# Kernel tuning notes

Hardware: AMD Instinct MI355X
Metric: run time of the kernel (lower is better)

The kernel has to match this reference:

```python
import jax, jax.numpy as jnp
import numpy as np

PI = float(np.pi)
LN_EPS = 1e-5
COS_EPS = 1e-6

D_HIDDEN, N_HEADS, D_HEAD, D_MLP = 1024, 16, 64, 4096
B, T = 4, 2048


def _xavier(key, shape):
    # torch xavier_uniform on 3D tensor: fan_in = shape[1]*shape[2]? torch uses
    # fan_in = shape[1] * receptive_field(shape[2:]), fan_out = shape[0] * rf.
    rf = 1
    for s in shape[2:]:
        rf *= s
    fan_in, fan_out = shape[1] * rf, shape[0] * rf
    bound = float(np.sqrt(6.0 / (fan_in + fan_out)))
    return jax.random.uniform(key, shape, jnp.float32, -bound, bound)


def setup_inputs() -> dict:
    key = jax.random.key(0)
    ks = jax.random.split(key, 10)
    x = jax.random.normal(ks[0], (B, T, D_HIDDEN), jnp.float32)
    W_Q = _xavier(ks[1], (N_HEADS, D_HIDDEN, 1))
    W_K = _xavier(ks[2], (N_HEADS, D_HIDDEN, 1))
    W_V = _xavier(ks[3], (N_HEADS, D_HIDDEN, D_HEAD))
    W_O = _xavier(ks[4], (D_HIDDEN, D_HEAD, N_HEADS))
    ln1_w = jnp.ones((D_HIDDEN,), jnp.float32)
    ln1_b = jnp.zeros((D_HIDDEN,), jnp.float32)
    ln2_w = jnp.ones((D_HIDDEN,), jnp.float32)
    ln2_b = jnp.zeros((D_HIDDEN,), jnp.float32)
    s1 = 1.0 / np.sqrt(D_HIDDEN)
    s2 = 1.0 / np.sqrt(D_MLP)
    W1 = jax.random.uniform(ks[5], (D_HIDDEN, D_MLP), jnp.float32, -s1, s1)
    b1 = jax.random.uniform(ks[6], (D_MLP,), jnp.float32, -s1, s1)
    W2 = jax.random.uniform(ks[7], (D_MLP, D_HIDDEN), jnp.float32, -s2, s2)
    b2 = jax.random.uniform(ks[8], (D_HIDDEN,), jnp.float32, -s2, s2)
    return {"x": x, "W_Q": W_Q, "W_K": W_K, "W_V": W_V, "W_O": W_O,
            "ln1_w": ln1_w, "ln1_b": ln1_b, "ln2_w": ln2_w, "ln2_b": ln2_b,
            "W1": W1, "b1": b1, "W2": W2, "b2": b2}


def _layer_norm(x, w, b):
    mu = jnp.mean(x, axis=-1, keepdims=True)
    var = jnp.mean(jnp.square(x - mu), axis=-1, keepdims=True)
    return (x - mu) * jax.lax.rsqrt(var + LN_EPS) * w + b


def _cos_attention(y, W_Q, W_K, W_V, W_O):
    q = jnp.einsum('btd,idh->btih', y, W_Q)  # (B,T,H,1)
    k = jnp.einsum('btd,idh->btih', y, W_K)  # (B,T,H,1)
    V = jnp.einsum('btd,idh->btih', y, W_V)  # (B,T,H,Dh)
    # use_tanh branch
    q = jnp.tanh(q) * (PI / 4)
    k = jnp.tanh(k) * (PI / 4)
    cos_k, sin_k = jnp.cos(k), jnp.sin(k)
    cos_KV = jnp.cumsum(cos_k * V, axis=1)
    sin_KV = jnp.cumsum(sin_k * V, axis=1)
    cos_Q, sin_Q = jnp.cos(q), jnp.sin(q)
    heads = cos_Q * cos_KV + sin_Q * sin_KV  # (B,T,H,Dh)
    # epsilon branch: normalizing denominator
    cos_K = jnp.cumsum(cos_k, axis=1)
    sin_K = jnp.cumsum(sin_k, axis=1)
    denom = cos_Q * cos_K + sin_Q * sin_K + COS_EPS  # (B,T,H,1)
    heads = heads / denom
    return jnp.einsum('dhi,btih->btd', W_O, heads)


def reference(x, W_Q, W_K, W_V, W_O, ln1_w, ln1_b, ln2_w, ln2_b, W1, b1, W2, b2):
    y = _layer_norm(x, ln1_w, ln1_b)
    x = x + _cos_attention(y, W_Q, W_K, W_V, W_O)
    y = _layer_norm(x, ln2_w, ln2_b)
    mlp = jnp.dot(jax.nn.gelu(jnp.dot(y, W1) + b1), W2) + b2
    return x + mlp
```

## Files before the change

kernel.cpp:

```cpp
#include <hip/hip_runtime.h>
#include <hip/hip_bf16.h>
#include <stdint.h>

typedef unsigned short u16;
typedef __attribute__((ext_vector_type(4))) unsigned int u32x4;
typedef __attribute__((ext_vector_type(8))) __bf16 bfx8;
typedef __attribute__((ext_vector_type(4))) float f32x4;

#define PI_F 3.14159265358979323846f

__device__ __forceinline__ float bf2f(u16 u) {
    unsigned v = ((unsigned)u) << 16; float f; __builtin_memcpy(&f, &v, 4); return f;
}
__device__ __forceinline__ u16 f2bf(float f) {
    unsigned u; __builtin_memcpy(&u, &f, 4);
    unsigned r = (u + 0x7fffu + ((u >> 16) & 1u)) >> 16; return (u16)r;
}

__device__ __forceinline__ void glds16(const u16* g, const u16* l) {
    __builtin_amdgcn_global_load_lds(
        (const __attribute__((address_space(1))) unsigned int*)(unsigned long long)g,
        (__attribute__((address_space(3))) unsigned int*)(unsigned int)(unsigned long long)l,
        16, 0, 0);
}

__global__ __launch_bounds__(256)
void tconv_kernel(const float* __restrict__ in, u16* __restrict__ out,
                  int R, int C, long inBatch, long outBatch)
{
    __shared__ float tile[64][65];
    const int tx = threadIdx.x & 63;
    const int ty = threadIdx.x >> 6;
    const int bc = blockIdx.x * 64;
    const int br = blockIdx.y * 64;
    const float* ip = in + (long)blockIdx.z * inBatch;
    u16* op = out + (long)blockIdx.z * outBatch;

    #pragma unroll
    for (int rr = ty; rr < 64; rr += 4) {
        int r = br + rr, c = bc + tx;
        tile[rr][tx] = (r < R && c < C) ? ip[(long)r * C + c] : 0.f;
    }
    __syncthreads();
    #pragma unroll
    for (int rr = ty; rr < 64; rr += 4) {
        int oc = bc + rr;
        int orr = br + tx;
        if (oc < C && orr < R)
            op[(long)oc * R + orr] = f2bf(tile[tx][rr]);
    }
}

template<bool DO_QK>
__global__ __launch_bounds__(256)
void ln_kernel(const float* __restrict__ X, const float* __restrict__ w,
               const float* __restrict__ b, u16* __restrict__ Ybf,
               const float* __restrict__ WQ, const float* __restrict__ WK,
               float* __restrict__ cqA, float* __restrict__ sqA,
               float* __restrict__ ckA, float* __restrict__ skA)
{
    __shared__ float yrow[1024];
    __shared__ float wsum[4], wsq[4];
    const int row = blockIdx.x;
    const int tid = threadIdx.x;
    const int lane = tid & 63;
    const int wv = tid >> 6;

    const float4 xv = ((const float4*)(X + (long)row * 1024))[tid];
    float s  = xv.x + xv.y + xv.z + xv.w;
    float sq = xv.x*xv.x + xv.y*xv.y + xv.z*xv.z + xv.w*xv.w;
    #pragma unroll
    for (int off = 32; off; off >>= 1) {
        s  += __shfl_down(s, off);
        sq += __shfl_down(sq, off);
    }
    if (lane == 0) { wsum[wv] = s; wsq[wv] = sq; }
    __syncthreads();
    const float ts = wsum[0] + wsum[1] + wsum[2] + wsum[3];
    const float tq = wsq[0] + wsq[1] + wsq[2] + wsq[3];
    const float mean = ts * (1.f / 1024.f);
    const float var  = tq * (1.f / 1024.f) - mean * mean;
    const float rstd = rsqrtf(var + 1e-5f);

    const float4 wv4 = ((const float4*)w)[tid];
    const float4 bv4 = ((const float4*)b)[tid];
    const float y0 = (xv.x - mean) * rstd * wv4.x + bv4.x;
    const float y1 = (xv.y - mean) * rstd * wv4.y + bv4.y;
    const float y2 = (xv.z - mean) * rstd * wv4.z + bv4.z;
    const float y3 = (xv.w - mean) * rstd * wv4.w + bv4.w;

    uint2 p;
    p.x = (unsigned)f2bf(y0) | ((unsigned)f2bf(y1) << 16);
    p.y = (unsigned)f2bf(y2) | ((unsigned)f2bf(y3) << 16);
    ((uint2*)(Ybf + (long)row * 1024))[tid] = p;

    if (DO_QK) {
        yrow[tid*4+0] = y0; yrow[tid*4+1] = y1;
        yrow[tid*4+2] = y2; yrow[tid*4+3] = y3;
        __syncthreads();
        #pragma unroll
        for (int i = 0; i < 4; ++i) {
            const int h = wv * 4 + i;
            const float* wqp = WQ + (long)h * 1024;
            const float* wkp = WK + (long)h * 1024;
            float dq = 0.f, dk = 0.f;
            #pragma unroll
            for (int j = 0; j < 16; ++j) {
                const float yv = yrow[lane + 64*j];
                dq = fmaf(yv, wqp[lane + 64*j], dq);
                dk = fmaf(yv, wkp[lane + 64*j], dk);
            }
            #pragma unroll
            for (int off = 32; off; off >>= 1) {
                dq += __shfl_down(dq, off);
                dk += __shfl_down(dk, off);
            }
            if (lane == 0) {
                const float aq = tanhf(dq) * (PI_F * 0.25f);
                const float ak = tanhf(dk) * (PI_F * 0.25f);
                float sv, cv;
                const long o = (long)h * 8192 + row;
                __sincosf(aq, &sv, &cv); cqA[o] = cv; sqA[o] = sv;
                __sincosf(ak, &sv, &cv); ckA[o] = cv; skA[o] = sv;
            }
        }
    }
}

__global__ __launch_bounds__(64)
void scan_kernel(const u16* __restrict__ V,
                 const float* __restrict__ cqA, const float* __restrict__ sqA,
                 const float* __restrict__ ckA, const float* __restrict__ skA,
                 u16* __restrict__ H)
{
    __shared__ u16 vt[64][64];
    __shared__ float lck[64], lsk[64], lrc[64], lrs[64];
    const int b = blockIdx.x >> 4;
    const int h = blockIdx.x & 15;
    const int lane = threadIdx.x;
    const long rowbase = (long)b * 2048;
    const long colbase = (long)h * 64;
    const long qbase = (long)h * 8192 + rowbase;

    float csum = 0.f, ssum = 0.f;
    float carry_c = 0.f, carry_s = 0.f;

    for (int ch = 0; ch < 32; ++ch) {
        const int t0 = ch * 64;
        __syncthreads();
        #pragma unroll
        for (int i = 0; i < 8; ++i) {
            const int tt = i * 8 + (lane >> 3);
            const int c0 = (lane & 7) * 8;
            *(u32x4*)&vt[tt][c0] =
                *(const u32x4*)(V + (rowbase + t0 + tt) * 1024 + colbase + c0);
        }
        {
            const float ck = ckA[qbase + t0 + lane];
            const float sk = skA[qbase + t0 + lane];
            const float cq = cqA[qbase + t0 + lane];
            const float sq = sqA[qbase + t0 + lane];
            float c = ck, sscan = sk;
            #pragma unroll
            for (int off = 1; off < 64; off <<= 1) {
                const float oc = __shfl_up(c, off);
                const float os = __shfl_up(sscan, off);
                if (lane >= off) { c += oc; sscan += os; }
            }
            const float cK = carry_c + c;
            const float sK = carry_s + sscan;
            carry_c += __shfl(c, 63);
            carry_s += __shfl(sscan, 63);
            const float denom = cq * cK + sq * sK + 1e-6f;
            lck[lane] = ck; lsk[lane] = sk;
            lrc[lane] = cq / denom; lrs[lane] = sq / denom;
        }
        __syncthreads();
        u16* outp = H + (rowbase + t0) * 1024 + colbase + lane;
        #pragma unroll 8
        for (int tt = 0; tt < 64; ++tt) {
            const float v = bf2f(vt[tt][lane]);
            csum = fmaf(lck[tt], v, csum);
            ssum = fmaf(lsk[tt], v, ssum);
            const float hv = lrc[tt] * csum + lrs[tt] * ssum;
            outp[(long)tt * 1024] = f2bf(hv);
        }
    }
}

template<int EPI>
__global__ __launch_bounds__(256, 2)
void gemm_bt(const u16* __restrict__ A, const u16* __restrict__ B,
             void* __restrict__ Cout, const float* __restrict__ res,
             const float* __restrict__ bias, int M, int N, int K)
{
    __shared__ u16 As[128 * 32];
    __shared__ u16 Bs[128 * 32];
    const int tid  = threadIdx.x;
    const int lane = tid & 63;
    const int wave = tid >> 6;
    const int wr = wave >> 1;
    const int wc = wave & 1;
    const int brow = blockIdx.y * 128;
    const int bcol = blockIdx.x * 128;

    const int srow = tid >> 2;
    const int cdst = tid & 3;
    const int csrc = (cdst - (srow >> 1)) & 3;
    const u16* Ag = A + (long)(brow + srow) * K + csrc * 8;
    const u16* Bg = B + (long)(bcol + srow) * K + csrc * 8;
    const u16* lA0 = &As[tid * 8];
    const u16* lA1 = &As[2048 + tid * 8];
    const u16* lB0 = &Bs[tid * 8];
    const u16* lB1 = &Bs[2048 + tid * 8];

    f32x4 acc[4][4];
    #pragma unroll
    for (int i = 0; i < 4; ++i)
        #pragma unroll
        for (int j = 0; j < 4; ++j) acc[i][j] = (f32x4){0.f, 0.f, 0.f, 0.f};

    const int rr = lane & 15;
    const int physc = ((lane >> 4) + (rr >> 1)) & 3;
    const char* Ab = (const char*)As;
    const char* Bb = (const char*)Bs;
    const int aoff0 = (wr * 64 + rr) * 64 + physc * 16;
    const int boff0 = (wc * 64 + rr) * 64 + physc * 16;

    const int KT = K >> 5;
    for (int kt = 0; kt < KT; ++kt) {
        const long ko = (long)kt * 32;
        __syncthreads();
        glds16(Ag + ko, lA0);
        glds16(Ag + ko + (long)64 * K, lA1);
        glds16(Bg + ko, lB0);
        glds16(Bg + ko + (long)64 * K, lB1);
        __syncthreads();
        bfx8 af[4], bfr[4];
        #pragma unroll
        for (int m = 0; m < 4; ++m)
            af[m] = *(const bfx8*)(Ab + aoff0 + m * (16 * 64));
        #pragma unroll
        for (int n = 0; n < 4; ++n)
            bfr[n] = *(const bfx8*)(Bb + boff0 + n * (16 * 64));
        #pragma unroll
        for (int m = 0; m < 4; ++m)
            #pragma unroll
            for (int n = 0; n < 4; ++n)
                acc[m][n] = __builtin_amdgcn_mfma_f32_16x16x32_bf16(
                    af[m], bfr[n], acc[m][n], 0, 0, 0);
    }

    const int crow0 = brow + wr * 64 + (lane >> 4) * 4;
    const int ccol0 = bcol + wc * 64 + (lane & 15);
    #pragma unroll
    for (int m = 0; m < 4; ++m) {
        #pragma unroll
        for (int n = 0; n < 4; ++n) {
            const int col = ccol0 + n * 16;
            #pragma unroll
            for (int r = 0; r < 4; ++r) {
                const int row = crow0 + m * 16 + r;
                const long idx = (long)row * N + col;
                const float v = acc[m][n][r];
                if (EPI == 0) {
                    ((u16*)Cout)[idx] = f2bf(v);
                } else if (EPI == 1) {
                    ((float*)Cout)[idx] = v + res[idx];
                } else if (EPI == 2) {
                    const float hh = v + bias[col];
                    const float g = 0.5f * hh *
                        (1.f + tanhf(0.7978845608028654f * (hh + 0.044715f * hh * hh * hh)));
                    ((u16*)Cout)[idx] = f2bf(g);
                } else {
                    ((float*)Cout)[idx] = v + res[idx] + bias[col];
                }
            }
        }
    }
}

extern "C" void kernel_launch(void* const* d_in, const int* in_sizes, int n_in,
                              void* d_out, int out_size, void* d_ws, size_t ws_size,
                              hipStream_t stream)
{
    (void)in_sizes; (void)n_in; (void)out_size; (void)ws_size;
    const float* x    = (const float*)d_in[0];
    const float* WQ   = (const float*)d_in[1];
    const float* WK   = (const float*)d_in[2];
    const float* WV   = (const float*)d_in[3];
    const float* WO   = (const float*)d_in[4];
    const float* ln1w = (const float*)d_in[5];
    const float* ln1b = (const float*)d_in[6];
    const float* ln2w = (const float*)d_in[7];
    const float* ln2b = (const float*)d_in[8];
    const float* W1   = (const float*)d_in[9];
    const float* b1   = (const float*)d_in[10];
    const float* W2   = (const float*)d_in[11];
    const float* b2   = (const float*)d_in[12];
    float* out = (float*)d_out;

    char* ws = (char*)d_ws;
    u16*   Ybf  = (u16*)(ws + 0);
    u16*   Vbf  = (u16*)(ws + 16777216);
    u16*   Hbf  = (u16*)(ws + 33554432);
    float* X2   = (float*)(ws + 50331648);
    u16*   H1   = (u16*)(ws + 83886080);
    u16*   WVT  = (u16*)(ws + 150994944);
    u16*   WOT  = (u16*)(ws + 153092096);
    u16*   W1T  = (u16*)(ws + 155189248);
    u16*   W2T  = (u16*)(ws + 163577856);
    float* CQ   = (float*)(ws + 171966464);
    float* SQ   = (float*)(ws + 172490752);
    float* CK   = (float*)(ws + 173015040);
    float* SK   = (float*)(ws + 173539328);

    tconv_kernel<<<dim3(1, 16, 16), 256, 0, stream>>>(WV, WVT, 1024, 64, 1024L*64, 64L*1024);
    tconv_kernel<<<dim3(1, 1, 1024), 256, 0, stream>>>(WO, WOT, 64, 16, 1024L, 1024L);
    tconv_kernel<<<dim3(64, 16, 1), 256, 0, stream>>>(W1, W1T, 1024, 4096, 0L, 0L);
    tconv_kernel<<<dim3(16, 64, 1), 256, 0, stream>>>(W2, W2T, 4096, 1024, 0L, 0L);

    ln_kernel<true><<<8192, 256, 0, stream>>>(x, ln1w, ln1b, Ybf, WQ, WK, CQ, SQ, CK, SK);

    gemm_bt<0><<<dim3(8, 64), 256, 0, stream>>>(Ybf, WVT, Vbf, nullptr, nullptr, 8192, 1024, 1024);

    scan_kernel<<<64, 64, 0, stream>>>(Vbf, CQ, SQ, CK, SK, Hbf);

    gemm_bt<1><<<dim3(8, 64), 256, 0, stream>>>(Hbf, WOT, X2, x, nullptr, 8192, 1024, 1024);

    ln_kernel<false><<<8192, 256, 0, stream>>>(X2, ln2w, ln2b, Ybf,
                                               nullptr, nullptr, nullptr, nullptr, nullptr, nullptr);

    gemm_bt<2><<<dim3(32, 64), 256, 0, stream>>>(Ybf, W1T, H1, nullptr, b1, 8192, 4096, 1024);

    gemm_bt<3><<<dim3(8, 64), 256, 0, stream>>>(H1, W2T, out, X2, b2, 8192, 1024, 4096);
}
```

Baseline: 559.4 us.

## Replace GEMM with 256-row tiled, 4-stage pipelined 512-thread kernel with XCD swizzle

```diff
diff --git a/kernel.cpp b/kernel.cpp
--- a/kernel.cpp
+++ b/kernel.cpp
@@ -188,75 +188,125 @@
     }
 }
 
-template<int EPI>
-__global__ __launch_bounds__(256, 2)
-void gemm_bt(const u16* __restrict__ A, const u16* __restrict__ B,
+template<int EPI, int BN>
+__global__ __launch_bounds__(512, 2)
+void gemm256(const u16* __restrict__ A, const u16* __restrict__ B,
              void* __restrict__ Cout, const float* __restrict__ res,
-             const float* __restrict__ bias, int M, int N, int K)
-{
-    __shared__ u16 As[128 * 32];
-    __shared__ u16 Bs[128 * 32];
+             const float* __restrict__ bias, int M, int N, int K, int nx)
+{
+    constexpr int NREP = BN / 64;
+    constexpr int GPT  = (BN == 256) ? 4 : 3;
+    __shared__ u16 As[4 * 256 * 32];
+    __shared__ u16 Bs[4 * BN * 32];
+
     const int tid  = threadIdx.x;
     const int lane = tid & 63;
     const int wave = tid >> 6;
-    const int wr = wave >> 1;
-    const int wc = wave & 1;
-    const int brow = blockIdx.y * 128;
-    const int bcol = blockIdx.x * 128;
+    const int wr = wave >> 2;
+    const int wc = wave & 3;
+
+    const int L = blockIdx.x;
+    const int xcd = L & 7;
+    const int q = L >> 3;
+    const int bx = q % nx;
+    const int by = (q / nx) * 8 + xcd;
+    const int brow = by * 256;
+    const int bcol = bx * BN;
 
     const int srow = tid >> 2;
-    const int cdst = tid & 3;
-    const int csrc = (cdst - (srow >> 1)) & 3;
-    const u16* Ag = A + (long)(brow + srow) * K + csrc * 8;
-    const u16* Bg = B + (long)(bcol + srow) * K + csrc * 8;
-    const u16* lA0 = &As[tid * 8];
-    const u16* lA1 = &As[2048 + tid * 8];
-    const u16* lB0 = &Bs[tid * 8];
-    const u16* lB1 = &Bs[2048 + tid * 8];
-
-    f32x4 acc[4][4];
-    #pragma unroll
-    for (int i = 0; i < 4; ++i)
-        #pragma unroll
-        for (int j = 0; j < 4; ++j) acc[i][j] = (f32x4){0.f, 0.f, 0.f, 0.f};
+    const int cd = tid & 3;
+    const int csrc = (cd - (srow >> 1)) & 3;
+    const u16* AgB = A + (long)(brow + srow) * K + csrc * 8;
+    const u16* BgB = B + (long)(bcol + srow) * K + csrc * 8;
+    const long rowK128 = (long)128 * K;
 
     const int rr = lane & 15;
     const int physc = ((lane >> 4) + (rr >> 1)) & 3;
+    const int aro = (wr * 128 + rr) * 64 + physc * 16;
+    const int bro = (wc * (BN / 4) + rr) * 64 + physc * 16;
+
+    f32x4 acc[8][NREP];
+    #pragma unroll
+    for (int m = 0; m < 8; ++m)
+        #pragma unroll
+        for (int n = 0; n < NREP; ++n) acc[m][n] = (f32x4){0.f, 0.f, 0.f, 0.f};
+
+    const int NT = K >> 5;
     const char* Ab = (const char*)As;
     const char* Bb = (const char*)Bs;
-    const int aoff0 = (wr * 64 + rr) * 64 + physc * 16;
-    const int boff0 = (wc * 64 + rr) * 64 + physc * 16;
-
-    const int KT = K >> 5;
-    for (int kt = 0; kt < KT; ++kt) {
-        const long ko = (long)kt * 32;
-        __syncthreads();
-        glds16(Ag + ko, lA0);
-        glds16(Ag + ko + (long)64 * K, lA1);
-        glds16(Bg + ko, lB0);
-        glds16(Bg + ko + (long)64 * K, lB1);
-        __syncthreads();
-        bfx8 af[4], bfr[4];
-        #pragma unroll
-        for (int m = 0; m < 4; ++m)
-            af[m] = *(const bfx8*)(Ab + aoff0 + m * (16 * 64));
-        #pragma unroll
-        for (int n = 0; n < 4; ++n)
-            bfr[n] = *(const bfx8*)(Bb + boff0 + n * (16 * 64));
-        #pragma unroll
-        for (int m = 0; m < 4; ++m)
-            #pragma unroll
-            for (int n = 0; n < 4; ++n)
+
+    #pragma unroll
+    for (int t = 0; t < 3; ++t) {
+        const int kof = t * 32;
+        glds16(AgB + kof,            &As[t * 8192 + tid * 8]);
+        glds16(AgB + kof + rowK128,  &As[t * 8192 + 4096 + tid * 8]);
+        glds16(BgB + kof,            &Bs[t * (BN * 32) + tid * 8]);
+        if constexpr (BN == 256)
+            glds16(BgB + kof + rowK128, &Bs[t * 8192 + 4096 + tid * 8]);
+    }
+    if constexpr (GPT == 4) asm volatile("s_waitcnt vmcnt(8)" ::: "memory");
+    else                    asm volatile("s_waitcnt vmcnt(6)" ::: "memory");
+    __builtin_amdgcn_s_barrier();
+
+    for (int kt = 0; kt < NT; ++kt) {
+        const int cur = kt & 3;
+        const int pf  = (kt + 3) & 3;
+        const int kof = ((kt + 3) < NT) ? (kt + 3) * 32 : 0;
+        const char* Abuf = Ab + cur * 16384;
+        const char* Bbuf = Bb + cur * (BN * 64);
+
+        bfx8 af[8], bf[NREP];
+        #pragma unroll
+        for (int m = 0; m < 8; ++m)
+            af[m] = *(const bfx8*)(Abuf + aro + m * 1024);
+        #pragma unroll
+        for (int n = 0; n < NREP / 2; ++n)
+            bf[n] = *(const bfx8*)(Bbuf + bro + n * 1024);
+        glds16(AgB + kof,           &As[pf * 8192 + tid * 8]);
+        glds16(AgB + kof + rowK128, &As[pf * 8192 + 4096 + tid * 8]);
+        __builtin_amdgcn_s_barrier();
+        asm volatile("s_waitcnt lgkmcnt(0)" ::: "memory");
+        __builtin_amdgcn_sched_barrier(0);
+        __builtin_amdgcn_s_setprio(1);
+        #pragma unroll
+        for (int m = 0; m < 8; ++m)
+            #pragma unroll
+            for (int n = 0; n < NREP / 2; ++n)
                 acc[m][n] = __builtin_amdgcn_mfma_f32_16x16x32_bf16(
-                    af[m], bfr[n], acc[m][n], 0, 0, 0);
-    }
-
-    const int crow0 = brow + wr * 64 + (lane >> 4) * 4;
-    const int ccol0 = bcol + wc * 64 + (lane & 15);
-    #pragma unroll
-    for (int m = 0; m < 4; ++m) {
-        #pragma unroll
-        for (int n = 0; n < 4; ++n) {
+                    af[m], bf[n], acc[m][n], 0, 0, 0);
+        __builtin_amdgcn_s_setprio(0);
+        __builtin_amdgcn_sched_barrier(0);
+        __builtin_amdgcn_s_barrier();
+
+        #pragma unroll
+        for (int n = NREP / 2; n < NREP; ++n)
+            bf[n] = *(const bfx8*)(Bbuf + bro + n * 1024);
+        glds16(BgB + kof, &Bs[pf * (BN * 32) + tid * 8]);
+        if constexpr (BN == 256)
+            glds16(BgB + kof + rowK128, &Bs[pf * 8192 + 4096 + tid * 8]);
+        __builtin_amdgcn_s_barrier();
+        asm volatile("s_waitcnt lgkmcnt(0)" ::: "memory");
+        __builtin_amdgcn_sched_barrier(0);
+        __builtin_amdgcn_s_setprio(1);
+        #pragma unroll
+        for (int m = 0; m < 8; ++m)
+            #pragma unroll
+            for (int n = NREP / 2; n < NREP; ++n)
+                acc[m][n] = __builtin_amdgcn_mfma_f32_16x16x32_bf16(
+                    af[m], bf[n], acc[m][n], 0, 0, 0);
+        __builtin_amdgcn_s_setprio(0);
+        __builtin_amdgcn_sched_barrier(0);
+        if constexpr (GPT == 4) asm volatile("s_waitcnt vmcnt(8)" ::: "memory");
+        else                    asm volatile("s_waitcnt vmcnt(6)" ::: "memory");
+        __builtin_amdgcn_s_barrier();
+    }
+
+    const int crow0 = brow + wr * 128 + (lane >> 4) * 4;
+    const int ccol0 = bcol + wc * (BN / 4) + rr;
+    #pragma unroll
+    for (int m = 0; m < 8; ++m) {
+        #pragma unroll
+        for (int n = 0; n < NREP; ++n) {
             const int col = ccol0 + n * 16;
             #pragma unroll
             for (int r = 0; r < 4; ++r) {
@@ -269,9 +319,10 @@
                     ((float*)Cout)[idx] = v + res[idx];
                 } else if (EPI == 2) {
                     const float hh = v + bias[col];
-                    const float g = 0.5f * hh *
-                        (1.f + tanhf(0.7978845608028654f * (hh + 0.044715f * hh * hh * hh)));
-                    ((u16*)Cout)[idx] = f2bf(g);
+                    const float z = 0.7978845608028654f * (hh + 0.044715f * hh * hh * hh);
+                    const float e = __expf(2.f * z);
+                    const float th = 1.f - 2.f / (e + 1.f);
+                    ((u16*)Cout)[idx] = f2bf(0.5f * hh * (1.f + th));
                 } else {
                     ((float*)Cout)[idx] = v + res[idx] + bias[col];
                 }
@@ -322,16 +373,16 @@
 
     ln_kernel<true><<<8192, 256, 0, stream>>>(x, ln1w, ln1b, Ybf, WQ, WK, CQ, SQ, CK, SK);
 
-    gemm_bt<0><<<dim3(8, 64), 256, 0, stream>>>(Ybf, WVT, Vbf, nullptr, nullptr, 8192, 1024, 1024);
+    gemm256<0, 128><<<256, 512, 0, stream>>>(Ybf, WVT, Vbf, nullptr, nullptr, 8192, 1024, 1024, 8);
 
     scan_kernel<<<64, 64, 0, stream>>>(Vbf, CQ, SQ, CK, SK, Hbf);
 
-    gemm_bt<1><<<dim3(8, 64), 256, 0, stream>>>(Hbf, WOT, X2, x, nullptr, 8192, 1024, 1024);
+    gemm256<1, 128><<<256, 512, 0, stream>>>(Hbf, WOT, X2, x, nullptr, 8192, 1024, 1024, 8);
 
     ln_kernel<false><<<8192, 256, 0, stream>>>(X2, ln2w, ln2b, Ybf,
                                                nullptr, nullptr, nullptr, nullptr, nullptr, nullptr);
 
-    gemm_bt<2><<<dim3(32, 64), 256, 0, stream>>>(Ybf, W1T, H1, nullptr, b1, 8192, 4096, 1024);
-
-    gemm_bt<3><<<dim3(8, 64), 256, 0, stream>>>(H1, W2T, out, X2, b2, 8192, 1024, 4096);
-}
+    gemm256<2, 256><<<512, 512, 0, stream>>>(Ybf, W1T, H1, nullptr, b1, 8192, 4096, 1024, 16);
+
+    gemm256<3, 128><<<256, 512, 0, stream>>>(H1, W2T, out, X2, b2, 8192, 1024, 4096, 8);
+}
```

Result: faster. 522.7 us (-6.6%).
